# Kernel tuning notes

Measured on AMD Instinct MI355X. Metric: run time of the kernel, lower is better.

## Reference

```python
import jax, jax.numpy as jnp
import numpy as np

N, E, G = 50000, 800000, 64
NODE_DIM, HID, HEADS, EDGE_DIM = 128, 256, 4, 2
LAYER_IN = [NODE_DIM, HID, HID]
LAYER_HEADS = [HEADS, HEADS, 1]
BN_EPS = 1e-5


def setup_inputs() -> dict:
    key = jax.random.key(0)
    ks = iter(jax.random.split(key, 80))
    def nrm(shape, s=0.05):
        return jax.random.normal(next(ks), shape, jnp.float32) * s
    inp = {}
    inp['x'] = jax.random.normal(next(ks), (N, NODE_DIM), jnp.float32)
    inp['edge_index'] = jax.random.randint(next(ks), (2, E), 0, N, jnp.int32)
    inp['edge_attr'] = jax.random.normal(next(ks), (E, EDGE_DIM), jnp.float32)
    inp['batch'] = jnp.sort(jax.random.randint(next(ks), (N,), 0, G, jnp.int32))
    for i in range(3):
        H = LAYER_HEADS[i]; C = HID // H
        inp[f'W{i}'] = nrm((LAYER_IN[i], H * C))
        inp[f'asrc{i}'] = nrm((H, C))
        inp[f'adst{i}'] = nrm((H, C))
        inp[f'We{i}'] = nrm((EDGE_DIM, H * C))
        inp[f'aedge{i}'] = nrm((H, C))
        inp[f'bconv{i}'] = jnp.zeros((HID,), jnp.float32)
        inp[f'bn{i}_g'] = jnp.ones((HID,), jnp.float32)
        inp[f'bn{i}_b'] = jnp.zeros((HID,), jnp.float32)
        inp[f'bn{i}_m'] = nrm((HID,), 0.01)
        inp[f'bn{i}_v'] = jnp.ones((HID,), jnp.float32)
    inp['Wskip'] = nrm((NODE_DIM, HID))
    inp['bskip'] = jnp.zeros((HID,), jnp.float32)
    inp['Wp1'] = nrm((2 * HID, HID))
    inp['bp1'] = jnp.zeros((HID,), jnp.float32)
    inp['Wp2'] = nrm((HID, 1))
    inp['bp2'] = jnp.zeros((1,), jnp.float32)
    return inp


def gat_conv(x, src, dst, ea, W, a_s, a_d, We, a_e, b, H, concat):
    n = x.shape[0]
    C = W.shape[1] // H
    h = (x @ W).reshape(n, H, C)                      # [N,H,C]
    # attention logits per edge (src/dst node terms + edge term)
    al = ((h * a_s).sum(-1)[src]
          + (h * a_d).sum(-1)[dst]
          + ((ea @ We).reshape(-1, H, C) * a_e).sum(-1))  # [Et,H]
    al = jax.nn.leaky_relu(al, 0.2)
    # segment softmax over destination nodes
    amax = jax.ops.segment_max(al, dst, num_segments=n)
    ex = jnp.exp(al - amax[dst])
    den = jax.ops.segment_sum(ex, dst, num_segments=n)
    alpha = ex / (den[dst] + 1e-16)
    out = jax.ops.segment_sum(h[src] * alpha[..., None], dst, num_segments=n)  # [N,H,C]
    out = out.reshape(n, H * C) if concat else out.mean(axis=1)
    return out + b


def _forward(x, edge_index, edge_attr, batch, layer_params, Wskip, bskip, Wp1, bp1, Wp2, bp2):
    n = x.shape[0]
    # add self-loops (PyG GATConv default), edge_attr filled with mean
    loop = jnp.arange(n, dtype=edge_index.dtype)
    src = jnp.concatenate([edge_index[0], loop])
    dst = jnp.concatenate([edge_index[1], loop])
    ea = jnp.concatenate([edge_attr, jnp.broadcast_to(edge_attr.mean(0), (n, edge_attr.shape[1]))], axis=0)
    identity = x
    for i, (W, a_s, a_d, We, a_e, b, g, be, rm, rv) in enumerate(layer_params):
        layer_identity = (identity @ Wskip + bskip) if i == 0 else identity
        concat = i < 2
        H = LAYER_HEADS[i]
        h = gat_conv(x, src, dst, ea, W, a_s, a_d, We, a_e, b, H, concat)
        h = (h - rm) * jax.lax.rsqrt(rv + BN_EPS) * g + be   # BatchNorm1d (eval)
        h = jax.nn.elu(h)
        x = h + layer_identity
        identity = x
    # global mean + max pool per graph
    counts = jnp.maximum(jax.ops.segment_sum(jnp.ones((n,), x.dtype), batch, num_segments=G), 1.0)
    mean_pool = jax.ops.segment_sum(x, batch, num_segments=G) / counts[:, None]
    max_pool = jax.ops.segment_max(x, batch, num_segments=G)
    emb = jnp.concatenate([mean_pool, max_pool], axis=1)      # [G, 2*HID]
    hmid = jax.nn.relu(emb @ Wp1 + bp1)
    return hmid @ Wp2 + bp2                                   # [G, 1]


def reference(x, edge_index, edge_attr, batch,
              W0, asrc0, adst0, We0, aedge0, bconv0, bn0_g, bn0_b, bn0_m, bn0_v,
              W1, asrc1, adst1, We1, aedge1, bconv1, bn1_g, bn1_b, bn1_m, bn1_v,
              W2, asrc2, adst2, We2, aedge2, bconv2, bn2_g, bn2_b, bn2_m, bn2_v,
              Wskip, bskip, Wp1, bp1, Wp2, bp2):
    layer_params = [
        (W0, asrc0, adst0, We0, aedge0, bconv0, bn0_g, bn0_b, bn0_m, bn0_v),
        (W1, asrc1, adst1, We1, aedge1, bconv1, bn1_g, bn1_b, bn1_m, bn1_v),
        (W2, asrc2, adst2, We2, aedge2, bconv2, bn2_g, bn2_b, bn2_m, bn2_v),
    ]
    return _forward(x, edge_index, edge_attr, batch, layer_params, Wskip, bskip, Wp1, bp1, Wp2, bp2)
```

## Files before the change

### kernel.cpp

```cpp
#include <hip/hip_runtime.h>
#include <cfloat>

#define Nn 50000
#define Ee 800000
#define Etot (Ee + Nn)
#define Gg 64
#define HIDc 256
#define BN_EPS 1e-5f

typedef unsigned int   uint32;
typedef unsigned short ushort16;
typedef short  bf16x8 __attribute__((ext_vector_type(8)));
typedef float  f32x4  __attribute__((ext_vector_type(4)));

__device__ inline ushort16 f2bf(float f) {
    uint32 u = __float_as_uint(f);
    u = (u + 0x7fffu + ((u >> 16) & 1u)) >> 16;
    return (ushort16)u;
}
__device__ inline uint32 pack2(float a, float b) {
    return (uint32)f2bf(a) | ((uint32)f2bf(b) << 16);
}
__device__ inline uint32 fenc(float f) {
    uint32 b = __float_as_uint(f);
    return (b & 0x80000000u) ? ~b : (b | 0x80000000u);
}
__device__ inline float fdec(uint32 u) {
    uint32 b = (u & 0x80000000u) ? (u & 0x7fffffffu) : ~u;
    return __uint_as_float(b);
}

__device__ inline long ws_index(int c, int k, int KB) {
    int cb = c >> 4, m = c & 15, kb = k >> 5, q = (k >> 3) & 3, e = k & 7;
    return (((long)(cb * KB + kb) * 64 + q * 16 + m) << 3) + e;
}

#define CVT4 (Nn * 128 / 4)
#define CVT_BLKS ((CVT4 + 255) / 256)
#define EBKS ((Etot + 255) / 256)
__global__ __launch_bounds__(256) void prep_kernel(
        const float* __restrict__ ea, float* __restrict__ ea_s,
        const float* __restrict__ We0, const float* __restrict__ ae0,
        const float* __restrict__ We1, const float* __restrict__ ae1,
        const float* __restrict__ We2, const float* __restrict__ ae2,
        float* __restrict__ M,
        const float* __restrict__ W0, const float* __restrict__ Wskip,
        const float* __restrict__ W1, const float* __restrict__ W2,
        ushort16* __restrict__ WtC, ushort16* __restrict__ Wt1,
        ushort16* __restrict__ Wt2,
        const float* __restrict__ x, ushort16* __restrict__ xbf,
        const int* __restrict__ ei, int* __restrict__ counts,
        const float* __restrict__ bc0, const float* __restrict__ g0,
        const float* __restrict__ b0, const float* __restrict__ m0,
        const float* __restrict__ v0,
        const float* __restrict__ bc1, const float* __restrict__ g1,
        const float* __restrict__ b1, const float* __restrict__ m1,
        const float* __restrict__ v1,
        const float* __restrict__ bc2, const float* __restrict__ g2,
        const float* __restrict__ b2, const float* __restrict__ m2,
        const float* __restrict__ v2,
        float* __restrict__ bnf) {
    int bid = blockIdx.x, t = threadIdx.x;
    if (bid < 256) {
        __shared__ float sh0[256], sh1[256];
        float s0 = 0.f, s1 = 0.f;
        for (int e = bid * 256 + t; e < Ee; e += 256 * 256) {
            s0 += ea[2 * e];
            s1 += ea[2 * e + 1];
        }
        sh0[t] = s0; sh1[t] = s1;
        __syncthreads();
        for (int off = 128; off > 0; off >>= 1) {
            if (t < off) { sh0[t] += sh0[t + off]; sh1[t] += sh1[t + off]; }
            __syncthreads();
        }
        if (t == 0) { atomicAdd(&ea_s[0], sh0[0]); atomicAdd(&ea_s[1], sh1[0]); }
    } else if (bid == 256) {
        if (t >= 18) return;
        int l = t < 8 ? 0 : (t < 16 ? 1 : 2);
        int r = t - l * 8;
        const float* We = (l == 0) ? We0 : (l == 1 ? We1 : We2);
        const float* ae = (l == 0) ? ae0 : (l == 1 ? ae1 : ae2);
        int Hl = (l < 2) ? 4 : 1;
        int Cl = 256 / Hl;
        int d = r / Hl, hh = r % Hl;
        float s = 0.f;
        for (int c = 0; c < Cl; ++c)
            s += We[d * 256 + hh * Cl + c] * ae[hh * Cl + c];
        M[l * 8 + r] = s;
    } else if (bid < 385) {
        int k = bid - 257;
        WtC[ws_index(t, k, 4)] = f2bf(W0[(long)k * 256 + t]);
    } else if (bid < 513) {
        int k = bid - 385;
        WtC[ws_index(256 + t, k, 4)] = f2bf(Wskip[(long)k * 256 + t]);
    } else if (bid < 769) {
        int k = bid - 513;
        Wt1[ws_index(t, k, 8)] = f2bf(W1[(long)k * 256 + t]);
    } else if (bid < 1025) {
        int k = bid - 769;
        Wt2[ws_index(t, k, 8)] = f2bf(W2[(long)k * 256 + t]);
    } else if (bid == 1025) {
        for (int ll = 0; ll < 3; ++ll) {
            const float* bc = ll == 0 ? bc0 : (ll == 1 ? bc1 : bc2);
            const float* gg = ll == 0 ? g0  : (ll == 1 ? g1  : g2);
            const float* bb = ll == 0 ? b0  : (ll == 1 ? b1  : b2);
            const float* mm = ll == 0 ? m0  : (ll == 1 ? m1  : m2);
            const float* vv = ll == 0 ? v0  : (ll == 1 ? v1  : v2);
            float s = gg[t] * rsqrtf(vv[t] + BN_EPS);
            bnf[ll * 512 + t]       = s;
            bnf[ll * 512 + 256 + t] = (bc[t] - mm[t]) * s + bb[t];
        }
    } else if (bid < 1026 + CVT_BLKS) {
        int i = (bid - 1026) * 256 + t;
        if (i < CVT4) {
            float4 v = *(const float4*)&x[i * 4];
            ushort4 o;
            o.x = f2bf(v.x); o.y = f2bf(v.y); o.z = f2bf(v.z); o.w = f2bf(v.w);
            *(ushort4*)&xbf[i * 4] = o;
        }
    } else {
        int e = (bid - 1026 - CVT_BLKS) * 256 + t;
        if (e < Etot) {
            int d = (e < Ee) ? ei[Ee + e] : (e - Ee);
            atomicAdd(&counts[d], 1);
        }
    }
}

__global__ void scan1_kernel(const int* __restrict__ in, int* __restrict__ inc,
                             int* __restrict__ bsums) {
    __shared__ int sh[256];
    int i = blockIdx.x * 256 + threadIdx.x;
    int v = (i < Nn) ? in[i] : 0;
    sh[threadIdx.x] = v;
    __syncthreads();
    for (int off = 1; off < 256; off <<= 1) {
        int t = ((int)threadIdx.x >= off) ? sh[threadIdx.x - off] : 0;
        __syncthreads();
        sh[threadIdx.x] += t;
        __syncthreads();
    }
    if (i < Nn) inc[i] = sh[threadIdx.x];
    if (threadIdx.x == 255) bsums[blockIdx.x] = sh[255];
}

__global__ void scan23_kernel(const int* __restrict__ inc, const int* __restrict__ bsums,
                              int* __restrict__ row_start, int* __restrict__ cursor, int nb) {
    __shared__ int sh[256];
    int b = blockIdx.x, t = threadIdx.x;
    sh[t] = (t < b && t < nb) ? bsums[t] : 0;
    __syncthreads();
    for (int off = 128; off > 0; off >>= 1) {
        if (t < off) sh[t] += sh[t + off];
        __syncthreads();
    }
    int base = sh[0];
    int i = b * 256 + t;
    if (i < Nn) {
        int v = inc[i] + base;
        row_start[i + 1] = v;
        cursor[i + 1] = v;
    }
    if (i == 0) { row_start[0] = 0; cursor[0] = 0; }
}

__global__ void scatter_kernel(const int* __restrict__ ei, const float* __restrict__ ea,
                               const float* __restrict__ ea_sum, int* __restrict__ cursor,
                               int* __restrict__ src_sorted, float* __restrict__ ea_sorted) {
    int e = blockIdx.x * blockDim.x + threadIdx.x;
    if (e >= Etot) return;
    int s, d; float e0, e1;
    if (e < Ee) {
        s = ei[e]; d = ei[Ee + e];
        e0 = ea[2 * e]; e1 = ea[2 * e + 1];
    } else {
        s = d = e - Ee;
        const float invE = 1.f / (float)Ee;
        e0 = ea_sum[0] * invE; e1 = ea_sum[1] * invE;
    }
    int pos = atomicAdd(&cursor[d], 1);
    src_sorted[pos] = s;
    ea_sorted[2 * pos]     = e0;
    ea_sorted[2 * pos + 1] = e1;
}

#define LDK 40
__global__ __launch_bounds__(256) void mfma_gemm_kernel(
        const ushort16* __restrict__ A,
        const ushort16* __restrict__ WS,
        uint32* __restrict__ outF,
        uint32* __restrict__ outS,
        const float* __restrict__ bskip,
        const float* __restrict__ a_s, const float* __restrict__ a_d,
        float* __restrict__ ssrc, float* __restrict__ sdst,
        int n, int K) {
    __shared__ ushort16 As[128 * LDK];
    const int t    = threadIdx.x;
    const int row0 = blockIdx.x * 128;
    const int c0   = blockIdx.y * 128;
    const bool isSkip = (outS != nullptr) && (c0 >= 256);
    const int cc0  = isSkip ? c0 - 256 : c0;
    const int wave = t >> 6, lane = t & 63;
    const int wr = wave >> 1, wc = wave & 1;
    const int l15 = lane & 15, quad = lane >> 4;
    const int KB = K >> 5;

    f32x4 acc[4][4];
#pragma unroll
    for (int j = 0; j < 4; ++j)
#pragma unroll
        for (int i = 0; i < 4; ++i) {
            acc[j][i][0] = 0.f; acc[j][i][1] = 0.f;
            acc[j][i][2] = 0.f; acc[j][i][3] = 0.f;
        }

    const int sm = t & 127;
    const int so = t >> 7;

    for (int k0 = 0; k0 < K; k0 += 32) {
        const int kb = k0 >> 5;
#pragma unroll
        for (int h = 0; h < 2; ++h) {
            int oct = so + 2 * h;
            int grow = row0 + sm;
            uint4 va = make_uint4(0, 0, 0, 0);
            if (grow < n) va = *(const uint4*)&A[(long)grow * K + k0 + 8 * oct];
            *(uint4*)&As[sm * LDK + 8 * oct] = va;
        }
        bf16x8 bfv[4];
#pragma unroll
        for (int j = 0; j < 4; ++j) {
            int cb = ((c0 + wc * 64) >> 4) + j;
            bfv[j] = *(const bf16x8*)&WS[(((long)cb * KB + kb) * 64 + lane) << 3];
        }
        __syncthreads();
        bf16x8 af[4];
#pragma unroll
        for (int i = 0; i < 4; ++i)
            af[i] = *(const bf16x8*)&As[(wr * 64 + i * 16 + l15) * LDK + quad * 8];
#pragma unroll
        for (int j = 0; j < 4; ++j)
#pragma unroll
            for (int i = 0; i < 4; ++i)
                acc[j][i] = __builtin_amdgcn_mfma_f32_16x16x32_bf16(
                    bfv[j], af[i], acc[j][i], 0, 0, 0);
        __syncthreads();
    }

    float4 bb[4];
#pragma unroll
    for (int j = 0; j < 4; ++j) {
        if (isSkip) bb[j] = *(const float4*)&bskip[cc0 + wc * 64 + j * 16 + quad * 4];
        else        bb[j] = make_float4(0.f, 0.f, 0.f, 0.f);
    }

    uint32* tgt = isSkip ? outS : outF;
#pragma unroll
    for (int i = 0; i < 4; ++i) {
        int row = row0 + wr * 64 + i * 16 + l15;
        if (row >= n) continue;
#pragma unroll
        for (int j = 0; j < 4; ++j) {
            int col = cc0 + wc * 64 + j * 16 + quad * 4;
            uint2 pk;
            pk.x = pack2(acc[j][i][0] + bb[j].x, acc[j][i][1] + bb[j].y);
            pk.y = pack2(acc[j][i][2] + bb[j].z, acc[j][i][3] + bb[j].w);
            *(uint2*)&tgt[(long)row * 128 + (col >> 1)] = pk;
        }
    }

    if (!isSkip && a_s != nullptr) {
        float4 asv[4], adv[4];
#pragma unroll
        for (int j = 0; j < 4; ++j) {
            int col = cc0 + wc * 64 + j * 16 + quad * 4;
            asv[j] = *(const float4*)&a_s[col];
            adv[j] = *(const float4*)&a_d[col];
        }
        const int part = (cc0 + wc * 64) >> 6;
#pragma unroll
        for (int i = 0; i < 4; ++i) {
            float ps = 0.f, pd = 0.f;
#pragma unroll
            for (int j = 0; j < 4; ++j) {
                ps += acc[j][i][0] * asv[j].x + acc[j][i][1] * asv[j].y
                    + acc[j][i][2] * asv[j].z + acc[j][i][3] * asv[j].w;
                pd += acc[j][i][0] * adv[j].x + acc[j][i][1] * adv[j].y
                    + acc[j][i][2] * adv[j].z + acc[j][i][3] * adv[j].w;
            }
            ps += __shfl_xor(ps, 16); ps += __shfl_xor(ps, 32);
            pd += __shfl_xor(pd, 16); pd += __shfl_xor(pd, 32);
            if (quad == 0) {
                int row = row0 + wr * 64 + i * 16 + l15;
                if (row < n) {
                    ssrc[row * 4 + part] = ps;
                    sdst[row * 4 + part] = pd;
                }
            }
        }
    }
}

template <int H>
__global__ __launch_bounds__(256) void agg_fused_kernel(
        const int* __restrict__ src_sorted, const int* __restrict__ row_start,
        const float* __restrict__ ea_sorted, const float* __restrict__ ssrc,
        const float* __restrict__ sdst, const float* __restrict__ M,
        const uint32* __restrict__ hbuf2,
        const float* __restrict__ bnS, const float* __restrict__ bnB,
        const uint32* __restrict__ identity2, uint32* __restrict__ out2,
        float* __restrict__ wspill) {
    __shared__ int   s_sh[4][64];
    __shared__ float w_sh[4][64 * H];
    const int wv = threadIdx.x >> 6;
    const int l  = threadIdx.x & 63;
    const int node = blockIdx.x * 4 + wv;
    if (node >= Nn) return;
    const int hh = (H == 4) ? (l >> 4) : 0;
    const int beg = row_start[node], end = row_start[node + 1];
    const int deg = end - beg;

    const int c = 4 * l;
    const float4 scv = *(const float4*)&bnS[c];
    const float4 sbv = *(const float4*)&bnB[c];
    const uint2  idu = *(const uint2*)&identity2[(long)node * 128 + 2 * l];

    float M0[H], M1[H], sd[H];
    {
        float4 sdv = *(const float4*)&sdst[node * 4];
        if (H == 4) { sd[0] = sdv.x; sd[1] = sdv.y; sd[2] = sdv.z; sd[3] = sdv.w; }
        else         sd[0] = sdv.x + sdv.y + sdv.z + sdv.w;
#pragma unroll
        for (int h = 0; h < H; ++h) { M0[h] = M[h]; M1[h] = M[H + h]; }
    }

    float a0 = 0.f, a1 = 0.f, a2 = 0.f, a3 = 0.f;

    auto gather = [&](int cnt) {
        const uint32 loff = (uint32)l << 3;
        for (int base = 0; base < cnt; base += 16) {
            int sk[16]; float wk[16]; uint2 f[16];
#pragma unroll
            for (int k = 0; k < 16; ++k) {
                sk[k] = s_sh[wv][base + k];
                wk[k] = w_sh[wv][(base + k) * H + hh];
            }
#pragma unroll
            for (int k = 0; k < 16; ++k)
                f[k] = *(const uint2*)((const char*)hbuf2 +
                                       (((uint32)sk[k] << 9) + loff));
#pragma unroll
            for (int k = 0; k < 16; ++k) {
                float ww = wk[k];
                a0 += ww * __uint_as_float(f[k].x << 16);
                a1 += ww * __uint_as_float(f[k].x & 0xffff0000u);
                a2 += ww * __uint_as_float(f[k].y << 16);
                a3 += ww * __uint_as_float(f[k].y & 0xffff0000u);
            }
        }
    };

    if (deg <= 64) {
        const int  el  = beg + l;
        const bool act = l < deg;
        const int  elc = min(el, end - 1);
        const int  s   = src_sorted[elc];
        const float e0 = ea_sorted[2 * elc], e1 = ea_sorted[2 * elc + 1];
        float4 sv = *(const float4*)&ssrc[s * 4];
        float lh[H], m[H];
#pragma unroll
        for (int h = 0; h < H; ++h) {
            float ss = (H == 4) ? ((const float*)&sv)[h]
                                : (sv.x + sv.y + sv.z + sv.w);
            float lg = ss + sd[h] + e0 * M0[h] + e1 * M1[h];
            lg = (lg > 0.f) ? lg : 0.2f * lg;
            lh[h] = lg;
            m[h]  = act ? lg : -FLT_MAX;
        }
#pragma unroll
        for (int h = 0; h < H; ++h) {
            m[h] = fmaxf(m[h], __shfl_xor(m[h], 1, 64));
            m[h] = fmaxf(m[h], __shfl_xor(m[h], 2, 64));
            m[h] = fmaxf(m[h], __shfl_xor(m[h], 4, 64));
            m[h] = fmaxf(m[h], __shfl_xor(m[h], 8, 64));
        }
        if (deg > 16) {
#pragma unroll
            for (int h = 0; h < H; ++h)
                m[h] = fmaxf(m[h], __shfl_xor(m[h], 16, 64));
        }
        if (deg > 32) {
#pragma unroll
            for (int h = 0; h < H; ++h)
                m[h] = fmaxf(m[h], __shfl_xor(m[h], 32, 64));
        }
        float ex[H], dn[H];
#pragma unroll
        for (int h = 0; h < H; ++h) {
            ex[h] = act ? __expf(lh[h] - m[h]) : 0.f;
            dn[h] = ex[h];
        }
#pragma unroll
        for (int h = 0; h < H; ++h) {
            dn[h] += __shfl_xor(dn[h], 1, 64);
            dn[h] += __shfl_xor(dn[h], 2, 64);
            dn[h] += __shfl_xor(dn[h], 4, 64);
            dn[h] += __shfl_xor(dn[h], 8, 64);
        }
        if (deg > 16) {
#pragma unroll
            for (int h = 0; h < H; ++h) dn[h] += __shfl_xor(dn[h], 16, 64);
        }
        if (deg > 32) {
#pragma unroll
            for (int h = 0; h < H; ++h) dn[h] += __shfl_xor(dn[h], 32, 64);
        }
        s_sh[wv][l] = s;
        if (H == 4) {
            float4 w4;
            w4.x = ex[0] * (1.f / (dn[0] + 1e-16f));
            w4.y = ex[1] * (1.f / (dn[1] + 1e-16f));
            w4.z = ex[2] * (1.f / (dn[2] + 1e-16f));
            w4.w = ex[3] * (1.f / (dn[3] + 1e-16f));
            *(float4*)&w_sh[wv][l * 4] = w4;
        } else {
            w_sh[wv][l] = ex[0] * (1.f / (dn[0] + 1e-16f));
        }
        asm volatile("s_waitcnt lgkmcnt(0)" ::: "memory");
        gather(deg);
    } else {
        float m[H], dn[H];
#pragma unroll
        for (int h = 0; h < H; ++h) { m[h] = -FLT_MAX; dn[h] = 0.f; }
        for (int cb = beg; cb < end; cb += 64) {
            int el = cb + l; bool act = el < end;
            int elc = min(el, end - 1);
            int s = src_sorted[elc];
            float e0 = ea_sorted[2 * elc], e1 = ea_sorted[2 * elc + 1];
            float4 sv = *(const float4*)&ssrc[s * 4];
#pragma unroll
            for (int h = 0; h < H; ++h) {
                float ss = (H == 4) ? ((const float*)&sv)[h]
                                    : (sv.x + sv.y + sv.z + sv.w);
                float lg = ss + sd[h] + e0 * M0[h] + e1 * M1[h];
                lg = (lg > 0.f) ? lg : 0.2f * lg;
                if (act) {
                    wspill[(long)el * H + h] = lg;
                    if (lg > m[h]) { dn[h] = dn[h] * __expf(m[h] - lg) + 1.f; m[h] = lg; }
                    else dn[h] += __expf(lg - m[h]);
                }
            }
        }
#pragma unroll
        for (int h = 0; h < H; ++h) {
#pragma unroll
            for (int off = 1; off < 64; off <<= 1) {
                float om = __shfl_xor(m[h], off, 64);
                float od = __shfl_xor(dn[h], off, 64);
                float nm = fmaxf(m[h], om);
                dn[h] = dn[h] * __expf(m[h] - nm) + od * __expf(om - nm);
                m[h] = nm;
            }
            dn[h] = 1.f / (dn[h] + 1e-16f);
        }
        for (int cb = beg; cb < end; cb += 64) {
            int el = cb + l; bool act = el < end;
            int elc = min(el, end - 1);
            s_sh[wv][l] = src_sorted[elc];
#pragma unroll
            for (int h = 0; h < H; ++h)
                w_sh[wv][l * H + h] =
                    act ? __expf(wspill[(long)el * H + h] - m[h]) * dn[h] : 0.f;
            asm volatile("s_waitcnt lgkmcnt(0)" ::: "memory");
            gather(min(64, end - cb));
            asm volatile("s_waitcnt lgkmcnt(0)" ::: "memory");
        }
    }

    float v0 = a0 * scv.x + sbv.x;
    float v1 = a1 * scv.y + sbv.y;
    float v2 = a2 * scv.z + sbv.z;
    float v3 = a3 * scv.w + sbv.w;
    v0 = (v0 > 0.f) ? v0 : (expf(v0) - 1.f);
    v1 = (v1 > 0.f) ? v1 : (expf(v1) - 1.f);
    v2 = (v2 > 0.f) ? v2 : (expf(v2) - 1.f);
    v3 = (v3 > 0.f) ? v3 : (expf(v3) - 1.f);
    v0 += __uint_as_float(idu.x << 16);
    v1 += __uint_as_float(idu.x & 0xffff0000u);
    v2 += __uint_as_float(idu.y << 16);
    v3 += __uint_as_float(idu.y & 0xffff0000u);
    uint2 o;
    o.x = pack2(v0, v1);
    o.y = pack2(v2, v3);
    *(uint2*)&out2[(long)node * 128 + 2 * l] = o;
}

#define POOL_ROWS 32
__global__ __launch_bounds__(128) void pool_kernel(
        const uint32* __restrict__ x2, const int* __restrict__ batch,
        float* __restrict__ psum, uint32* __restrict__ pmax, float* __restrict__ pcnt) {
    int c2 = threadIdx.x;
    int n0 = blockIdx.x * POOL_ROWS;
    if (n0 >= Nn) return;
    int n1 = min(n0 + POOL_ROWS, Nn);
    int cur = batch[n0];
    float s0 = 0.f, s1 = 0.f, m0 = -FLT_MAX, m1 = -FLT_MAX;
    int cnt = 0;
    int c = 2 * c2;
    for (int i = n0; i < n1; ++i) {
        int g = batch[i];
        if (g != cur) {
            atomicAdd(&psum[cur * 256 + c], s0);
            atomicAdd(&psum[cur * 256 + c + 1], s1);
            atomicMax(&pmax[cur * 256 + c], fenc(m0));
            atomicMax(&pmax[cur * 256 + c + 1], fenc(m1));
            if (c2 == 0) atomicAdd(&pcnt[cur], (float)cnt);
            cur = g; s0 = s1 = 0.f; m0 = m1 = -FLT_MAX; cnt = 0;
        }
        uint32 u = x2[(long)i * 128 + c2];
        float lo = __uint_as_float(u << 16);
        float hi = __uint_as_float(u & 0xffff0000u);
        s0 += lo; s1 += hi;
        m0 = fmaxf(m0, lo); m1 = fmaxf(m1, hi);
        ++cnt;
    }
    atomicAdd(&psum[cur * 256 + c], s0);
    atomicAdd(&psum[cur * 256 + c + 1], s1);
    atomicMax(&pmax[cur * 256 + c], fenc(m0));
    atomicMax(&pmax[cur * 256 + c + 1], fenc(m1));
    if (c2 == 0) atomicAdd(&pcnt[cur], (float)cnt);
}

__global__ __launch_bounds__(256) void mlp_kernel(
        const float* __restrict__ psum, const uint32* __restrict__ pmax,
        const float* __restrict__ pcnt, const float* __restrict__ Wp1,
        const float* __restrict__ bp1, const float* __restrict__ Wp2,
        const float* __restrict__ bp2, float* __restrict__ out) {
    int g = blockIdx.x;
    int j = threadIdx.x;
    float inv = 1.f / fmaxf(pcnt[g], 1.f);
    float acc = bp1[j];
    for (int k = 0; k < 256; ++k)
        acc += (psum[g * 256 + k] * inv) * Wp1[k * 256 + j];
    for (int k = 0; k < 256; ++k)
        acc += fdec(pmax[g * 256 + k]) * Wp1[(256 + k) * 256 + j];
    float v = fmaxf(acc, 0.f) * Wp2[j];
    __shared__ float red[256];
    red[j] = v;
    __syncthreads();
    for (int off = 128; off > 0; off >>= 1) {
        if (j < off) red[j] += red[j + off];
        __syncthreads();
    }
    if (j == 0) out[g] = red[0] + bp2[0];
}

extern "C" void kernel_launch(void* const* d_in, const int* in_sizes, int n_in,
                              void* d_out, int out_size, void* d_ws, size_t ws_size,
                              hipStream_t stream) {
    const float* x   = (const float*)d_in[0];
    const int*   ei  = (const int*)d_in[1];
    const float* ea  = (const float*)d_in[2];
    const int*   bat = (const int*)d_in[3];
    auto LP = [&](int l, int j) { return (const float*)d_in[4 + l * 10 + j]; };
    const float* Wskip = (const float*)d_in[34];
    const float* bskip = (const float*)d_in[35];
    const float* Wp1   = (const float*)d_in[36];
    const float* bp1   = (const float*)d_in[37];
    const float* Wp2   = (const float*)d_in[38];
    const float* bp2   = (const float*)d_in[39];
    float* out = (float*)d_out;

    char* p = (char*)d_ws;
    auto alloc = [&](size_t bytes) { void* r = (void*)p; p += (bytes + 255) & ~(size_t)255; return r; };
    uint32*   hbuf2  = (uint32*)alloc((size_t)Nn * 256 * 2);
    uint32*   skipbf = (uint32*)alloc((size_t)Nn * 128 * 4);
    uint32*   resA   = (uint32*)alloc((size_t)Nn * 128 * 4);
    uint32*   resB   = (uint32*)alloc((size_t)Nn * 128 * 4);
    ushort16* xbf    = (ushort16*)alloc((size_t)Nn * 128 * 2);
    float*    wbuf   = (float*)alloc((size_t)Etot * 4 * 4);
    float*    ea_sorted = (float*)alloc((size_t)Etot * 2 * 4);
    float*    ssrc   = (float*)alloc((size_t)Nn * 4 * 4);
    float*    sdst   = (float*)alloc((size_t)Nn * 4 * 4);
    int*      counts = (int*)alloc((size_t)Nn * 4);
    int*      incb   = (int*)alloc((size_t)Nn * 4);
    int*      row_start = (int*)alloc((size_t)(Nn + 1) * 4);
    int*      cursor    = (int*)alloc((size_t)(Nn + 1) * 4);
    int*      src_sorted = (int*)alloc((size_t)Etot * 4);
    int*      bsums  = (int*)alloc(256 * 4);
    float*    ea_s   = (float*)alloc(2 * 4);
    float*    Mbuf   = (float*)alloc(32 * 4);
    float*    bnf    = (float*)alloc((size_t)3 * 512 * 4);
    ushort16* WtC    = (ushort16*)alloc((size_t)512 * 128 * 2);
    ushort16* Wt1    = (ushort16*)alloc((size_t)256 * 256 * 2);
    ushort16* Wt2    = (ushort16*)alloc((size_t)256 * 256 * 2);
    float*    psum   = (float*)alloc((size_t)Gg * 256 * 4);
    uint32*   pmax   = (uint32*)alloc((size_t)Gg * 256 * 4);
    float*    pcnt   = (float*)alloc((size_t)Gg * 4);

    const int nb = (Nn + 255) / 256;

    hipMemsetAsync(counts, 0, (size_t)Nn * 4, stream);
    hipMemsetAsync(ea_s, 0, 8, stream);
    hipMemsetAsync(psum, 0, (size_t)Gg * 256 * 4 * 2 + (size_t)Gg * 4, stream);

    prep_kernel<<<1026 + CVT_BLKS + EBKS, 256, 0, stream>>>(
        ea, ea_s, LP(0,3), LP(0,4), LP(1,3), LP(1,4), LP(2,3), LP(2,4), Mbuf,
        LP(0,0), Wskip, LP(1,0), LP(2,0), WtC, Wt1, Wt2, x, xbf, ei, counts,
        LP(0,5), LP(0,6), LP(0,7), LP(0,8), LP(0,9),
        LP(1,5), LP(1,6), LP(1,7), LP(1,8), LP(1,9),
        LP(2,5), LP(2,6), LP(2,7), LP(2,8), LP(2,9),
        bnf);

    scan1_kernel<<<nb, 256, 0, stream>>>(counts, incb, bsums);
    scan23_kernel<<<nb, 256, 0, stream>>>(incb, bsums, row_start, cursor, nb);
    scatter_kernel<<<EBKS, 256, 0, stream>>>(ei, ea, ea_s, cursor, src_sorted, ea_sorted);

    {
        dim3 g0((Nn + 127) / 128, 4);
        mfma_gemm_kernel<<<g0, 256, 0, stream>>>(
            xbf, WtC, hbuf2, skipbf, bskip,
            LP(0,1), LP(0,2), ssrc, sdst, Nn, 128);
    }

    const uint32* lid[3] = { skipbf, resA, resB };
    uint32*       lou[3] = { resA, resB, resA };
    const ushort16* lain[3] = { nullptr, (ushort16*)resA, (ushort16*)resB };
    const ushort16* lwt[3]  = { nullptr, Wt1, Wt2 };
    for (int l = 0; l < 3; ++l) {
        if (l > 0) {
            dim3 gl((Nn + 127) / 128, 2);
            mfma_gemm_kernel<<<gl, 256, 0, stream>>>(
                lain[l], lwt[l], hbuf2, nullptr, nullptr,
                LP(l,1), LP(l,2), ssrc, sdst, Nn, 256);
        }
        if (l < 2)
            agg_fused_kernel<4><<<(Nn + 3) / 4, 256, 0, stream>>>(
                src_sorted, row_start, ea_sorted, ssrc, sdst, Mbuf + l * 8,
                hbuf2, bnf + l * 512, bnf + l * 512 + 256,
                lid[l], lou[l], wbuf);
        else
            agg_fused_kernel<1><<<(Nn + 3) / 4, 256, 0, stream>>>(
                src_sorted, row_start, ea_sorted, ssrc, sdst, Mbuf + l * 8,
                hbuf2, bnf + l * 512, bnf + l * 512 + 256,
                lid[l], lou[l], wbuf);
    }

    pool_kernel<<<(Nn + POOL_ROWS - 1) / POOL_ROWS, 128, 0, stream>>>(resA, bat, psum, pmax, pcnt);
    mlp_kernel<<<Gg, 256, 0, stream>>>(psum, pmax, pcnt, Wp1, bp1, Wp2, bp2, out);
}
```

Before: 623.1 us.

## Process four nodes per wavefront with software-pipelined metadata prefetch in aggregation

Each wavefront in the fused GAT aggregation kernel now handles four consecutive destination nodes instead of one. While it works on the current node, it prefetches the next nodes' row bounds, source indices, edge attributes, dst scores, identity rows and source scores two stages ahead. The aim is to hide the latency of the dependent index-then-score loads between nodes and to cut the grid size by four. The cost is more registers per thread, which can lower occupancy, and more serial work per wavefront, which can worsen load balance across wavefronts.

Result: no change. 626.5 us (+0.6%).

```diff
diff --git a/kernel.cpp b/kernel.cpp
--- a/kernel.cpp
+++ b/kernel.cpp
@@ -302,6 +302,9 @@
     }
 }
 
+#define AGG_P 4
+struct MetaS { int s, beg, end; float e0, e1; float4 sd; uint2 idu; };
+
 template <int H>
 __global__ __launch_bounds__(256) void agg_fused_kernel(
         const int* __restrict__ src_sorted, const int* __restrict__ row_start,
@@ -315,28 +318,31 @@
     __shared__ float w_sh[4][64 * H];
     const int wv = threadIdx.x >> 6;
     const int l  = threadIdx.x & 63;
-    const int node = blockIdx.x * 4 + wv;
-    if (node >= Nn) return;
+    const int nbase = (blockIdx.x * 4 + wv) * AGG_P;
+    if (nbase >= Nn) return;
     const int hh = (H == 4) ? (l >> 4) : 0;
-    const int beg = row_start[node], end = row_start[node + 1];
-    const int deg = end - beg;
-
     const int c = 4 * l;
     const float4 scv = *(const float4*)&bnS[c];
     const float4 sbv = *(const float4*)&bnB[c];
-    const uint2  idu = *(const uint2*)&identity2[(long)node * 128 + 2 * l];
-
-    float M0[H], M1[H], sd[H];
-    {
-        float4 sdv = *(const float4*)&sdst[node * 4];
-        if (H == 4) { sd[0] = sdv.x; sd[1] = sdv.y; sd[2] = sdv.z; sd[3] = sdv.w; }
-        else         sd[0] = sdv.x + sdv.y + sdv.z + sdv.w;
-#pragma unroll
-        for (int h = 0; h < H; ++h) { M0[h] = M[h]; M1[h] = M[H + h]; }
-    }
-
-    float a0 = 0.f, a1 = 0.f, a2 = 0.f, a3 = 0.f;
-
+    float M0[H], M1[H];
+#pragma unroll
+    for (int h = 0; h < H; ++h) { M0[h] = M[h]; M1[h] = M[H + h]; }
+
+    const int rsv = row_start[min(nbase + min(l, AGG_P), Nn)];
+
+    auto issue1 = [&](int j, MetaS& mt) {
+        mt.beg = __shfl(rsv, j, 64);
+        mt.end = __shfl(rsv, j + 1, 64);
+        int elc = min(mt.beg + l, mt.end - 1);
+        mt.s = src_sorted[elc];
+        float2 ev = *(const float2*)&ea_sorted[2 * elc];
+        mt.e0 = ev.x; mt.e1 = ev.y;
+        int ndc = min(nbase + j, Nn - 1);
+        mt.sd = *(const float4*)&sdst[ndc * 4];
+        mt.idu = *(const uint2*)&identity2[(long)ndc * 128 + 2 * l];
+    };
+
+    float a0, a1, a2, a3;
     auto gather = [&](int cnt) {
         const uint32 loff = (uint32)l << 3;
         for (int base = 0; base < cnt; base += 16) {
@@ -361,139 +367,165 @@
         }
     };
 
-    if (deg <= 64) {
-        const int  el  = beg + l;
-        const bool act = l < deg;
-        const int  elc = min(el, end - 1);
-        const int  s   = src_sorted[elc];
-        const float e0 = ea_sorted[2 * elc], e1 = ea_sorted[2 * elc + 1];
-        float4 sv = *(const float4*)&ssrc[s * 4];
-        float lh[H], m[H];
-#pragma unroll
-        for (int h = 0; h < H; ++h) {
-            float ss = (H == 4) ? ((const float*)&sv)[h]
-                                : (sv.x + sv.y + sv.z + sv.w);
-            float lg = ss + sd[h] + e0 * M0[h] + e1 * M1[h];
-            lg = (lg > 0.f) ? lg : 0.2f * lg;
-            lh[h] = lg;
-            m[h]  = act ? lg : -FLT_MAX;
-        }
-#pragma unroll
-        for (int h = 0; h < H; ++h) {
-            m[h] = fmaxf(m[h], __shfl_xor(m[h], 1, 64));
-            m[h] = fmaxf(m[h], __shfl_xor(m[h], 2, 64));
-            m[h] = fmaxf(m[h], __shfl_xor(m[h], 4, 64));
-            m[h] = fmaxf(m[h], __shfl_xor(m[h], 8, 64));
-        }
-        if (deg > 16) {
-#pragma unroll
-            for (int h = 0; h < H; ++h)
-                m[h] = fmaxf(m[h], __shfl_xor(m[h], 16, 64));
-        }
-        if (deg > 32) {
-#pragma unroll
-            for (int h = 0; h < H; ++h)
-                m[h] = fmaxf(m[h], __shfl_xor(m[h], 32, 64));
-        }
-        float ex[H], dn[H];
-#pragma unroll
-        for (int h = 0; h < H; ++h) {
-            ex[h] = act ? __expf(lh[h] - m[h]) : 0.f;
-            dn[h] = ex[h];
-        }
-#pragma unroll
-        for (int h = 0; h < H; ++h) {
-            dn[h] += __shfl_xor(dn[h], 1, 64);
-            dn[h] += __shfl_xor(dn[h], 2, 64);
-            dn[h] += __shfl_xor(dn[h], 4, 64);
-            dn[h] += __shfl_xor(dn[h], 8, 64);
-        }
-        if (deg > 16) {
-#pragma unroll
-            for (int h = 0; h < H; ++h) dn[h] += __shfl_xor(dn[h], 16, 64);
-        }
-        if (deg > 32) {
-#pragma unroll
-            for (int h = 0; h < H; ++h) dn[h] += __shfl_xor(dn[h], 32, 64);
-        }
-        s_sh[wv][l] = s;
-        if (H == 4) {
-            float4 w4;
-            w4.x = ex[0] * (1.f / (dn[0] + 1e-16f));
-            w4.y = ex[1] * (1.f / (dn[1] + 1e-16f));
-            w4.z = ex[2] * (1.f / (dn[2] + 1e-16f));
-            w4.w = ex[3] * (1.f / (dn[3] + 1e-16f));
-            *(float4*)&w_sh[wv][l * 4] = w4;
+    MetaS mA, mB, mC;
+    float4 svA, svB;
+    issue1(0, mA);
+    if (AGG_P > 1) issue1(1, mB);
+    svA = *(const float4*)&ssrc[mA.s * 4];
+
+#pragma unroll
+    for (int j = 0; j < AGG_P; ++j) {
+        const int node = nbase + j;
+        if (node >= Nn) break;
+        if (j + 2 < AGG_P) issue1(j + 2, mC);
+        const int deg = mA.end - mA.beg;
+        a0 = a1 = a2 = a3 = 0.f;
+
+        if (deg <= 64) {
+            const bool act = l < deg;
+            float sd[H];
+            if (H == 4) {
+                sd[0] = mA.sd.x; sd[1] = mA.sd.y; sd[2] = mA.sd.z; sd[3] = mA.sd.w;
+            } else {
+                sd[0] = mA.sd.x + mA.sd.y + mA.sd.z + mA.sd.w;
+            }
+            float lh[H], m[H];
+#pragma unroll
+            for (int h = 0; h < H; ++h) {
+                float ss = (H == 4) ? ((const float*)&svA)[h]
+                                    : (svA.x + svA.y + svA.z + svA.w);
+                float lg = ss + sd[h] + mA.e0 * M0[h] + mA.e1 * M1[h];
+                lg = (lg > 0.f) ? lg : 0.2f * lg;
+                lh[h] = lg;
+                m[h]  = act ? lg : -FLT_MAX;
+            }
+#pragma unroll
+            for (int h = 0; h < H; ++h) {
+                m[h] = fmaxf(m[h], __shfl_xor(m[h], 1, 64));
+                m[h] = fmaxf(m[h], __shfl_xor(m[h], 2, 64));
+                m[h] = fmaxf(m[h], __shfl_xor(m[h], 4, 64));
+                m[h] = fmaxf(m[h], __shfl_xor(m[h], 8, 64));
+            }
+            if (deg > 16) {
+#pragma unroll
+                for (int h = 0; h < H; ++h)
+                    m[h] = fmaxf(m[h], __shfl_xor(m[h], 16, 64));
+            }
+            if (deg > 32) {
+#pragma unroll
+                for (int h = 0; h < H; ++h)
+                    m[h] = fmaxf(m[h], __shfl_xor(m[h], 32, 64));
+            }
+            float ex[H], dn[H];
+#pragma unroll
+            for (int h = 0; h < H; ++h) {
+                ex[h] = act ? __expf(lh[h] - m[h]) : 0.f;
+                dn[h] = ex[h];
+            }
+#pragma unroll
+            for (int h = 0; h < H; ++h) {
+                dn[h] += __shfl_xor(dn[h], 1, 64);
+                dn[h] += __shfl_xor(dn[h], 2, 64);
+                dn[h] += __shfl_xor(dn[h], 4, 64);
+                dn[h] += __shfl_xor(dn[h], 8, 64);
+            }
+            if (deg > 16) {
+#pragma unroll
+                for (int h = 0; h < H; ++h) dn[h] += __shfl_xor(dn[h], 16, 64);
+            }
+            if (deg > 32) {
+#pragma unroll
+                for (int h = 0; h < H; ++h) dn[h] += __shfl_xor(dn[h], 32, 64);
+            }
+            s_sh[wv][l] = mA.s;
+            if (H == 4) {
+                float4 w4;
+                w4.x = ex[0] * (1.f / (dn[0] + 1e-16f));
+                w4.y = ex[1] * (1.f / (dn[1] + 1e-16f));
+                w4.z = ex[2] * (1.f / (dn[2] + 1e-16f));
+                w4.w = ex[3] * (1.f / (dn[3] + 1e-16f));
+                *(float4*)&w_sh[wv][l * 4] = w4;
+            } else {
+                w_sh[wv][l] = ex[0] * (1.f / (dn[0] + 1e-16f));
+            }
+            if (j + 1 < AGG_P) svB = *(const float4*)&ssrc[mB.s * 4];
+            asm volatile("s_waitcnt lgkmcnt(0)" ::: "memory");
+            gather(deg);
         } else {
-            w_sh[wv][l] = ex[0] * (1.f / (dn[0] + 1e-16f));
-        }
-        asm volatile("s_waitcnt lgkmcnt(0)" ::: "memory");
-        gather(deg);
-    } else {
-        float m[H], dn[H];
-#pragma unroll
-        for (int h = 0; h < H; ++h) { m[h] = -FLT_MAX; dn[h] = 0.f; }
-        for (int cb = beg; cb < end; cb += 64) {
-            int el = cb + l; bool act = el < end;
-            int elc = min(el, end - 1);
-            int s = src_sorted[elc];
-            float e0 = ea_sorted[2 * elc], e1 = ea_sorted[2 * elc + 1];
-            float4 sv = *(const float4*)&ssrc[s * 4];
+            if (j + 1 < AGG_P) svB = *(const float4*)&ssrc[mB.s * 4];
+            float sd[H];
+            if (H == 4) {
+                sd[0] = mA.sd.x; sd[1] = mA.sd.y; sd[2] = mA.sd.z; sd[3] = mA.sd.w;
+            } else {
+                sd[0] = mA.sd.x + mA.sd.y + mA.sd.z + mA.sd.w;
+            }
+            float m[H], dn[H];
+#pragma unroll
+            for (int h = 0; h < H; ++h) { m[h] = -FLT_MAX; dn[h] = 0.f; }
+            for (int cb = mA.beg; cb < mA.end; cb += 64) {
+                int el = cb + l; bool act2 = el < mA.end;
+                int elc = min(el, mA.end - 1);
+                int s = src_sorted[elc];
+                float e0 = ea_sorted[2 * elc], e1 = ea_sorted[2 * elc + 1];
+                float4 sv = *(const float4*)&ssrc[s * 4];
+#pragma unroll
+                for (int h = 0; h < H; ++h) {
+                    float ss = (H == 4) ? ((const float*)&sv)[h]
+                                        : (sv.x + sv.y + sv.z + sv.w);
+                    float lg = ss + sd[h] + e0 * M0[h] + e1 * M1[h];
+                    lg = (lg > 0.f) ? lg : 0.2f * lg;
+                    if (act2) {
+                        wspill[(long)el * H + h] = lg;
+                        if (lg > m[h]) { dn[h] = dn[h] * __expf(m[h] - lg) + 1.f; m[h] = lg; }
+                        else dn[h] += __expf(lg - m[h]);
+                    }
+                }
+            }
 #pragma unroll
             for (int h = 0; h < H; ++h) {
-                float ss = (H == 4) ? ((const float*)&sv)[h]
-                                    : (sv.x + sv.y + sv.z + sv.w);
-                float lg = ss + sd[h] + e0 * M0[h] + e1 * M1[h];
-                lg = (lg > 0.f) ? lg : 0.2f * lg;
-                if (act) {
-                    wspill[(long)el * H + h] = lg;
-                    if (lg > m[h]) { dn[h] = dn[h] * __expf(m[h] - lg) + 1.f; m[h] = lg; }
-                    else dn[h] += __expf(lg - m[h]);
+#pragma unroll
+                for (int off = 1; off < 64; off <<= 1) {
+                    float om = __shfl_xor(m[h], off, 64);
+                    float od = __shfl_xor(dn[h], off, 64);
+                    float nm = fmaxf(m[h], om);
+                    dn[h] = dn[h] * __expf(m[h] - nm) + od * __expf(om - nm);
+                    m[h] = nm;
                 }
-            }
-        }
-#pragma unroll
-        for (int h = 0; h < H; ++h) {
-#pragma unroll
-            for (int off = 1; off < 64; off <<= 1) {
-                float om = __shfl_xor(m[h], off, 64);
-                float od = __shfl_xor(dn[h], off, 64);
-                float nm = fmaxf(m[h], om);
-                dn[h] = dn[h] * __expf(m[h] - nm) + od * __expf(om - nm);
-                m[h] = nm;
-            }
-            dn[h] = 1.f / (dn[h] + 1e-16f);
-        }
-        for (int cb = beg; cb < end; cb += 64) {
-            int el = cb + l; bool act = el < end;
-            int elc = min(el, end - 1);
-            s_sh[wv][l] = src_sorted[elc];
-#pragma unroll
-            for (int h = 0; h < H; ++h)
-                w_sh[wv][l * H + h] =
-                    act ? __expf(wspill[(long)el * H + h] - m[h]) * dn[h] : 0.f;
-            asm volatile("s_waitcnt lgkmcnt(0)" ::: "memory");
-            gather(min(64, end - cb));
-            asm volatile("s_waitcnt lgkmcnt(0)" ::: "memory");
-        }
-    }
-
-    float v0 = a0 * scv.x + sbv.x;
-    float v1 = a1 * scv.y + sbv.y;
-    float v2 = a2 * scv.z + sbv.z;
-    float v3 = a3 * scv.w + sbv.w;
-    v0 = (v0 > 0.f) ? v0 : (expf(v0) - 1.f);
-    v1 = (v1 > 0.f) ? v1 : (expf(v1) - 1.f);
-    v2 = (v2 > 0.f) ? v2 : (expf(v2) - 1.f);
-    v3 = (v3 > 0.f) ? v3 : (expf(v3) - 1.f);
-    v0 += __uint_as_float(idu.x << 16);
-    v1 += __uint_as_float(idu.x & 0xffff0000u);
-    v2 += __uint_as_float(idu.y << 16);
-    v3 += __uint_as_float(idu.y & 0xffff0000u);
-    uint2 o;
-    o.x = pack2(v0, v1);
-    o.y = pack2(v2, v3);
-    *(uint2*)&out2[(long)node * 128 + 2 * l] = o;
+                dn[h] = 1.f / (dn[h] + 1e-16f);
+            }
+            for (int cb = mA.beg; cb < mA.end; cb += 64) {
+                int el = cb + l; bool act2 = el < mA.end;
+                int elc = min(el, mA.end - 1);
+                s_sh[wv][l] = src_sorted[elc];
+#pragma unroll
+                for (int h = 0; h < H; ++h)
+                    w_sh[wv][l * H + h] =
+                        act2 ? __expf(wspill[(long)el * H + h] - m[h]) * dn[h] : 0.f;
+                asm volatile("s_waitcnt lgkmcnt(0)" ::: "memory");
+                gather(min(64, mA.end - cb));
+                asm volatile("s_waitcnt lgkmcnt(0)" ::: "memory");
+            }
+        }
+
+        float v0 = a0 * scv.x + sbv.x;
+        float v1 = a1 * scv.y + sbv.y;
+        float v2 = a2 * scv.z + sbv.z;
+        float v3 = a3 * scv.w + sbv.w;
+        v0 = (v0 > 0.f) ? v0 : (expf(v0) - 1.f);
+        v1 = (v1 > 0.f) ? v1 : (expf(v1) - 1.f);
+        v2 = (v2 > 0.f) ? v2 : (expf(v2) - 1.f);
+        v3 = (v3 > 0.f) ? v3 : (expf(v3) - 1.f);
+        v0 += __uint_as_float(mA.idu.x << 16);
+        v1 += __uint_as_float(mA.idu.x & 0xffff0000u);
+        v2 += __uint_as_float(mA.idu.y << 16);
+        v3 += __uint_as_float(mA.idu.y & 0xffff0000u);
+        uint2 o;
+        o.x = pack2(v0, v1);
+        o.y = pack2(v2, v3);
+        *(uint2*)&out2[(long)node * 128 + 2 * l] = o;
+
+        mA = mB; svA = svB; mB = mC;
+    }
 }
 
 #define POOL_ROWS 32
@@ -624,6 +656,7 @@
             LP(0,1), LP(0,2), ssrc, sdst, Nn, 128);
     }
 
+    const int agrid = (Nn + 4 * AGG_P - 1) / (4 * AGG_P);
     const uint32* lid[3] = { skipbf, resA, resB };
     uint32*       lou[3] = { resA, resB, resA };
     const ushort16* lain[3] = { nullptr, (ushort16*)resA, (ushort16*)resB };
@@ -636,12 +669,12 @@
                 LP(l,1), LP(l,2), ssrc, sdst, Nn, 256);
         }
         if (l < 2)
-            agg_fused_kernel<4><<<(Nn + 3) / 4, 256, 0, stream>>>(
+            agg_fused_kernel<4><<<agrid, 256, 0, stream>>>(
                 src_sorted, row_start, ea_sorted, ssrc, sdst, Mbuf + l * 8,
                 hbuf2, bnf + l * 512, bnf + l * 512 + 256,
                 lid[l], lou[l], wbuf);
         else
-            agg_fused_kernel<1><<<(Nn + 3) / 4, 256, 0, stream>>>(
+            agg_fused_kernel<1><<<agrid, 256, 0, stream>>>(
                 src_sorted, row_start, ea_sorted, ssrc, sdst, Mbuf + l * 8,
                 hbuf2, bnf + l * 512, bnf + l * 512 + 256,
                 lid[l], lou[l], wbuf);
```
